# Performance work log

Hardware: AMD Instinct MI355X
Metric: run time of the kernel (lower is better)

Reference implementation:

```python
import jax, jax.numpy as jnp
import numpy as np

N = 65536        # nodes
E = 1048576      # edges (avg degree 16)
IN, HID, OUT = 128, 64, 64


def setup_inputs() -> dict:
    key = jax.random.key(0)
    ks = jax.random.split(key, 6)
    x = jax.random.normal(ks[0], (N, IN), jnp.float32)
    edge_index = jax.random.randint(ks[1], (2, E), 0, N, jnp.int32)
    # Glorot-style init as in PyG GCNConv
    W1 = jax.random.normal(ks[2], (IN, HID), jnp.float32) * (1.0 / np.sqrt(IN))
    b1 = jnp.zeros((HID,), jnp.float32)
    W2 = jax.random.normal(ks[3], (HID, OUT), jnp.float32) * (1.0 / np.sqrt(HID))
    b2 = jnp.zeros((OUT,), jnp.float32)
    return {"x": x, "edge_index": edge_index, "W1": W1, "b1": b1, "W2": W2, "b2": b2}


def _gcn_conv(h, src, dst, dinv_sqrt, W, b):
    # PyG GCNConv: transform, then D^-1/2 A_hat D^-1/2 aggregation (A_hat has self-loops)
    h = h @ W                                   # [N, F_out]
    norm = dinv_sqrt[src] * dinv_sqrt[dst]      # [E+N]
    msg = h[src] * norm[:, None]                # gather + scale
    return jax.ops.segment_sum(msg, dst, num_segments=N) + b


def reference(x, edge_index, W1, b1, W2, b2):
    loops = jnp.arange(N, dtype=edge_index.dtype)
    src = jnp.concatenate([edge_index[0], loops])   # [E+N] with self-loops
    dst = jnp.concatenate([edge_index[1], loops])
    deg = jax.ops.segment_sum(jnp.ones_like(dst, x.dtype), dst, num_segments=N)
    dinv_sqrt = jax.lax.rsqrt(deg)                  # deg >= 1 thanks to self-loops
    h = jax.nn.relu(_gcn_conv(x, src, dst, dinv_sqrt, W1, b1))
    return _gcn_conv(h, src, dst, dinv_sqrt, W2, b2)
```

## Files before the change

kernel.cpp:

```cpp
#include <hip/hip_runtime.h>
#include <hip/hip_fp16.h>


#define N_NODES 65536
#define E_EDGES 1048576
#define F_IN    128
#define F_HID   64
#define CAPSH   6

__global__ __launch_bounds__(256) void k_fill(
        const int* __restrict__ src, const int* __restrict__ dst,
        int* __restrict__ cnt, unsigned short* __restrict__ csr) {
    int g     = blockIdx.x & 7;
    int chunk = blockIdx.x >> 3;
    int i     = chunk * blockDim.x + threadIdx.x;
    int4 d = ((const int4*)dst)[i];
#pragma unroll
    for (int k = 0; k < 4; ++k) {
        int dv = k == 0 ? d.x : k == 1 ? d.y : k == 2 ? d.z : d.w;
        if ((dv >> 13) == g) {
            int pos = atomicAdd(&cnt[dv], 1);
            csr[(dv << CAPSH) + pos] = (unsigned short)src[4 * i + k];
        }
    }
}

__device__ inline unsigned int pack_h2(float a, float b) {
    __half2 h = __floats2half2_rn(a, b);
    return *(unsigned int*)&h;
}

template <int F_K>
__global__ __launch_bounds__(256) void k_gemm_scale(
        const float* __restrict__ h, const float* __restrict__ W,
        const int* __restrict__ cnt, __half* __restrict__ P) {
    int wave = __builtin_amdgcn_readfirstlane(threadIdx.x >> 6);
    int lane = threadIdx.x & 63;
    int v = blockIdx.x * 64 + lane;
    const float4* hr = (const float4*)(h + (size_t)v * F_K);
    float4 acc[4];
#pragma unroll
    for (int j = 0; j < 4; ++j) acc[j] = make_float4(0.f, 0.f, 0.f, 0.f);
#pragma unroll 4
    for (int kb = 0; kb < F_K / 4; ++kb) {
        float4 hv = hr[kb];
#pragma unroll
        for (int r = 0; r < 4; ++r) {
            float hk = r == 0 ? hv.x : r == 1 ? hv.y : r == 2 ? hv.z : hv.w;
            const float4* Wr = (const float4*)(W + (size_t)(kb * 4 + r) * 64 + (wave << 4));
#pragma unroll
            for (int j = 0; j < 4; ++j) {
                float4 w = Wr[j];
                acc[j].x = fmaf(hk, w.x, acc[j].x);
                acc[j].y = fmaf(hk, w.y, acc[j].y);
                acc[j].z = fmaf(hk, w.z, acc[j].z);
                acc[j].w = fmaf(hk, w.w, acc[j].w);
            }
        }
    }
    float s = rsqrtf((float)cnt[v] + 1.0f);
    __half* Pr = P + (size_t)v * 64 + (wave << 4);
    uint4 q0, q1;
    q0.x = pack_h2(acc[0].x * s, acc[0].y * s);
    q0.y = pack_h2(acc[0].z * s, acc[0].w * s);
    q0.z = pack_h2(acc[1].x * s, acc[1].y * s);
    q0.w = pack_h2(acc[1].z * s, acc[1].w * s);
    q1.x = pack_h2(acc[2].x * s, acc[2].y * s);
    q1.y = pack_h2(acc[2].z * s, acc[2].w * s);
    q1.z = pack_h2(acc[3].x * s, acc[3].y * s);
    q1.w = pack_h2(acc[3].z * s, acc[3].w * s);
    ((uint4*)Pr)[0] = q0;
    ((uint4*)Pr)[1] = q1;
}

__device__ inline float4 h4_to_f4(uint2 q) {
    __half2 a = *(__half2*)&q.x;
    __half2 b = *(__half2*)&q.y;
    float2 fa = __half22float2(a), fb = __half22float2(b);
    return make_float4(fa.x, fa.y, fb.x, fb.y);
}

template <bool RELU>
__global__ void k_aggregate(const __half* __restrict__ P,
                            const unsigned short* __restrict__ csr,
                            const int* __restrict__ cnt, const float* __restrict__ b,
                            float* __restrict__ out) {
    int lane = threadIdx.x & 63;
    int sub  = lane >> 4;
    int col4 = lane & 15;
    int wave  = (blockIdx.x * blockDim.x + threadIdx.x) >> 6;
    int nwave = (gridDim.x * blockDim.x) >> 6;
    float4 bias = ((const float4*)b)[col4];
    for (int v = wave; v < N_NODES; v += nwave) {
        int c   = cnt[v];
        int beg = v << CAPSH;
        float4 acc = make_float4(0.f, 0.f, 0.f, 0.f);
        if (sub == 0) {
            uint2 q = ((const uint2*)(P + (size_t)v * 64))[col4];
            acc = h4_to_f4(q);
        }
        for (int i = 0; i < c; i += 4) {
            int e = i + sub;
            if (e < c) {
                int s = csr[beg + e];
                uint2 q = ((const uint2*)(P + (size_t)s * 64))[col4];
                float4 p = h4_to_f4(q);
                acc.x += p.x; acc.y += p.y; acc.z += p.z; acc.w += p.w;
            }
        }
        acc.x += __shfl_xor(acc.x, 16); acc.y += __shfl_xor(acc.y, 16);
        acc.z += __shfl_xor(acc.z, 16); acc.w += __shfl_xor(acc.w, 16);
        acc.x += __shfl_xor(acc.x, 32); acc.y += __shfl_xor(acc.y, 32);
        acc.z += __shfl_xor(acc.z, 32); acc.w += __shfl_xor(acc.w, 32);
        if (lane < 16) {
            float s = rsqrtf((float)c + 1.0f);
            float4 o;
            o.x = s * acc.x + bias.x;
            o.y = s * acc.y + bias.y;
            o.z = s * acc.z + bias.z;
            o.w = s * acc.w + bias.w;
            if (RELU) {
                o.x = o.x > 0.f ? o.x : 0.f;
                o.y = o.y > 0.f ? o.y : 0.f;
                o.z = o.z > 0.f ? o.z : 0.f;
                o.w = o.w > 0.f ? o.w : 0.f;
            }
            ((float4*)(out + (size_t)v * 64))[col4] = o;
        }
    }
}

extern "C" void kernel_launch(void* const* d_in, const int* in_sizes, int n_in,
                              void* d_out, int out_size, void* d_ws, size_t ws_size,
                              hipStream_t stream) {
    const float* x   = (const float*)d_in[0];
    const int*   ei  = (const int*)d_in[1];
    const float* W1  = (const float*)d_in[2];
    const float* b1  = (const float*)d_in[3];
    const float* W2  = (const float*)d_in[4];
    const float* b2  = (const float*)d_in[5];
    float*       out = (float*)d_out;

    const int* src = ei;
    const int* dst = ei + E_EDGES;

    int*            cnt = (int*)d_ws;
    unsigned short* csr = (unsigned short*)(cnt + N_NODES);
    __half*         P   = (__half*)(csr + ((size_t)N_NODES << CAPSH));
    float*          H   = out;

    hipMemsetAsync(cnt, 0, N_NODES * sizeof(int), stream);
    k_fill<<<(E_EDGES / 4 / 256) * 8, 256, 0, stream>>>(src, dst, cnt, csr);

    k_gemm_scale<F_IN><<<N_NODES / 64, 256, 0, stream>>>(x, W1, cnt, P);
    k_aggregate<true><<<4096, 256, 0, stream>>>(P, csr, cnt, b1, H);

    k_gemm_scale<F_HID><<<N_NODES / 64, 256, 0, stream>>>(H, W2, cnt, P);
    k_aggregate<false><<<4096, 256, 0, stream>>>(P, csr, cnt, b2, out);
}
```

Baseline: 236.7 us.

## Fuse first GEMM with CSR fill kernel and precompute inverse sqrt degrees

Merges the first-layer GEMM and the edge bucketing fill into one launch, with blocks split by index so the GEMM no longer waits on the degree count. Because degrees are unknown when the GEMM runs, the first aggregation now scales each source row by a gathered dinv value. A small kernel precomputes dinv once for both layers, and the aggregation loop is unrolled by two edges. This trades an extra per-edge dinv gather and an extra launch for concurrency between the compute-bound GEMM and the atomic-heavy fill.

```diff
diff --git a/kernel.cpp b/kernel.cpp
--- a/kernel.cpp
+++ b/kernel.cpp
@@ -7,36 +7,28 @@
 #define F_IN    128
 #define F_HID   64
 #define CAPSH   6
-
-__global__ __launch_bounds__(256) void k_fill(
-        const int* __restrict__ src, const int* __restrict__ dst,
-        int* __restrict__ cnt, unsigned short* __restrict__ csr) {
-    int g     = blockIdx.x & 7;
-    int chunk = blockIdx.x >> 3;
-    int i     = chunk * blockDim.x + threadIdx.x;
-    int4 d = ((const int4*)dst)[i];
-#pragma unroll
-    for (int k = 0; k < 4; ++k) {
-        int dv = k == 0 ? d.x : k == 1 ? d.y : k == 2 ? d.z : d.w;
-        if ((dv >> 13) == g) {
-            int pos = atomicAdd(&cnt[dv], 1);
-            csr[(dv << CAPSH) + pos] = (unsigned short)src[4 * i + k];
-        }
-    }
-}
+#define GEMM1_BLOCKS (N_NODES / 64)
+#define FILL_BLOCKS  ((E_EDGES / 4 / 256) * 8)
 
 __device__ inline unsigned int pack_h2(float a, float b) {
     __half2 h = __floats2half2_rn(a, b);
     return *(unsigned int*)&h;
 }
 
-template <int F_K>
-__global__ __launch_bounds__(256) void k_gemm_scale(
-        const float* __restrict__ h, const float* __restrict__ W,
-        const int* __restrict__ cnt, __half* __restrict__ P) {
+__device__ inline float4 h4_to_f4(uint2 q) {
+    __half2 a = *(__half2*)&q.x;
+    __half2 b = *(__half2*)&q.y;
+    float2 fa = __half22float2(a), fb = __half22float2(b);
+    return make_float4(fa.x, fa.y, fb.x, fb.y);
+}
+
+template <int F_K, bool SCALED>
+__device__ inline void gemm_body(const float* __restrict__ h, const float* __restrict__ W,
+                                 const float* __restrict__ dinv, __half* __restrict__ P,
+                                 int bid) {
     int wave = __builtin_amdgcn_readfirstlane(threadIdx.x >> 6);
     int lane = threadIdx.x & 63;
-    int v = blockIdx.x * 64 + lane;
+    int v = bid * 64 + lane;
     const float4* hr = (const float4*)(h + (size_t)v * F_K);
     float4 acc[4];
 #pragma unroll
@@ -58,7 +50,7 @@
             }
         }
     }
-    float s = rsqrtf((float)cnt[v] + 1.0f);
+    float s = SCALED ? dinv[v] : 1.0f;
     __half* Pr = P + (size_t)v * 64 + (wave << 4);
     uint4 q0, q1;
     q0.x = pack_h2(acc[0].x * s, acc[0].y * s);
@@ -73,18 +65,47 @@
     ((uint4*)Pr)[1] = q1;
 }
 
-__device__ inline float4 h4_to_f4(uint2 q) {
-    __half2 a = *(__half2*)&q.x;
-    __half2 b = *(__half2*)&q.y;
-    float2 fa = __half22float2(a), fb = __half22float2(b);
-    return make_float4(fa.x, fa.y, fb.x, fb.y);
+__global__ __launch_bounds__(256) void k_fused(
+        const float* __restrict__ x, const float* __restrict__ W1,
+        __half* __restrict__ P,
+        const int* __restrict__ src, const int* __restrict__ dst,
+        int* __restrict__ cnt, unsigned short* __restrict__ csr) {
+    if (blockIdx.x < GEMM1_BLOCKS) {
+        gemm_body<F_IN, false>(x, W1, nullptr, P, blockIdx.x);
+    } else {
+        int fb    = blockIdx.x - GEMM1_BLOCKS;
+        int g     = fb & 7;
+        int chunk = fb >> 3;
+        int i     = chunk * blockDim.x + threadIdx.x;
+        int4 d = ((const int4*)dst)[i];
+#pragma unroll
+        for (int k = 0; k < 4; ++k) {
+            int dv = k == 0 ? d.x : k == 1 ? d.y : k == 2 ? d.z : d.w;
+            if ((dv >> 13) == g) {
+                int pos = atomicAdd(&cnt[dv], 1);
+                csr[(dv << CAPSH) + pos] = (unsigned short)src[4 * i + k];
+            }
+        }
+    }
 }
 
-template <bool RELU>
+__global__ void k_dinv(const int* __restrict__ cnt, float* __restrict__ dinv) {
+    int v = blockIdx.x * blockDim.x + threadIdx.x;
+    if (v < N_NODES) dinv[v] = rsqrtf((float)cnt[v] + 1.0f);
+}
+
+template <int F_K, bool SCALED>
+__global__ __launch_bounds__(256) void k_gemm(
+        const float* __restrict__ h, const float* __restrict__ W,
+        const float* __restrict__ dinv, __half* __restrict__ P) {
+    gemm_body<F_K, SCALED>(h, W, dinv, P, blockIdx.x);
+}
+
+template <bool RELU, bool SRCSCALE>
 __global__ void k_aggregate(const __half* __restrict__ P,
                             const unsigned short* __restrict__ csr,
-                            const int* __restrict__ cnt, const float* __restrict__ b,
-                            float* __restrict__ out) {
+                            const int* __restrict__ cnt, const float* __restrict__ dinv,
+                            const float* __restrict__ b, float* __restrict__ out) {
     int lane = threadIdx.x & 63;
     int sub  = lane >> 4;
     int col4 = lane & 15;
@@ -92,20 +113,33 @@
     int nwave = (gridDim.x * blockDim.x) >> 6;
     float4 bias = ((const float4*)b)[col4];
     for (int v = wave; v < N_NODES; v += nwave) {
-        int c   = cnt[v];
-        int beg = v << CAPSH;
+        int c    = cnt[v];
+        float dv = dinv[v];
+        int beg  = v << CAPSH;
         float4 acc = make_float4(0.f, 0.f, 0.f, 0.f);
         if (sub == 0) {
             uint2 q = ((const uint2*)(P + (size_t)v * 64))[col4];
-            acc = h4_to_f4(q);
+            float4 p = h4_to_f4(q);
+            float sc = SRCSCALE ? dv : 1.0f;
+            acc.x = sc * p.x; acc.y = sc * p.y; acc.z = sc * p.z; acc.w = sc * p.w;
         }
-        for (int i = 0; i < c; i += 4) {
-            int e = i + sub;
-            if (e < c) {
-                int s = csr[beg + e];
-                uint2 q = ((const uint2*)(P + (size_t)s * 64))[col4];
-                float4 p = h4_to_f4(q);
-                acc.x += p.x; acc.y += p.y; acc.z += p.z; acc.w += p.w;
+        for (int i = 0; i < c; i += 8) {
+            int e0 = i + sub, e1 = i + sub + 4;
+            if (e0 < c) {
+                int s0 = csr[beg + e0];
+                float f0 = SRCSCALE ? dinv[s0] : 1.0f;
+                uint2 q0 = ((const uint2*)(P + (size_t)s0 * 64))[col4];
+                float4 p0 = h4_to_f4(q0);
+                acc.x = fmaf(f0, p0.x, acc.x); acc.y = fmaf(f0, p0.y, acc.y);
+                acc.z = fmaf(f0, p0.z, acc.z); acc.w = fmaf(f0, p0.w, acc.w);
+            }
+            if (e1 < c) {
+                int s1 = csr[beg + e1];
+                float f1 = SRCSCALE ? dinv[s1] : 1.0f;
+                uint2 q1 = ((const uint2*)(P + (size_t)s1 * 64))[col4];
+                float4 p1 = h4_to_f4(q1);
+                acc.x = fmaf(f1, p1.x, acc.x); acc.y = fmaf(f1, p1.y, acc.y);
+                acc.z = fmaf(f1, p1.z, acc.z); acc.w = fmaf(f1, p1.w, acc.w);
             }
         }
         acc.x += __shfl_xor(acc.x, 16); acc.y += __shfl_xor(acc.y, 16);
@@ -113,12 +147,11 @@
         acc.x += __shfl_xor(acc.x, 32); acc.y += __shfl_xor(acc.y, 32);
         acc.z += __shfl_xor(acc.z, 32); acc.w += __shfl_xor(acc.w, 32);
         if (lane < 16) {
-            float s = rsqrtf((float)c + 1.0f);
             float4 o;
-            o.x = s * acc.x + bias.x;
-            o.y = s * acc.y + bias.y;
-            o.z = s * acc.z + bias.z;
-            o.w = s * acc.w + bias.w;
+            o.x = dv * acc.x + bias.x;
+            o.y = dv * acc.y + bias.y;
+            o.z = dv * acc.z + bias.z;
+            o.w = dv * acc.w + bias.w;
             if (RELU) {
                 o.x = o.x > 0.f ? o.x : 0.f;
                 o.y = o.y > 0.f ? o.y : 0.f;
@@ -144,17 +177,19 @@
     const int* src = ei;
     const int* dst = ei + E_EDGES;
 
-    int*            cnt = (int*)d_ws;
-    unsigned short* csr = (unsigned short*)(cnt + N_NODES);
-    __half*         P   = (__half*)(csr + ((size_t)N_NODES << CAPSH));
-    float*          H   = out;
+    int*            cnt  = (int*)d_ws;
+    float*          dinv = (float*)(cnt + N_NODES);
+    unsigned short* csr  = (unsigned short*)(dinv + N_NODES);
+    __half*         P    = (__half*)(csr + ((size_t)N_NODES << CAPSH));
+    float*          H    = out;
 
     hipMemsetAsync(cnt, 0, N_NODES * sizeof(int), stream);
-    k_fill<<<(E_EDGES / 4 / 256) * 8, 256, 0, stream>>>(src, dst, cnt, csr);
 
-    k_gemm_scale<F_IN><<<N_NODES / 64, 256, 0, stream>>>(x, W1, cnt, P);
-    k_aggregate<true><<<4096, 256, 0, stream>>>(P, csr, cnt, b1, H);
+    k_fused<<<GEMM1_BLOCKS + FILL_BLOCKS, 256, 0, stream>>>(x, W1, P, src, dst, cnt, csr);
+    k_dinv<<<N_NODES / 256, 256, 0, stream>>>(cnt, dinv);
 
-    k_gemm_scale<F_HID><<<N_NODES / 64, 256, 0, stream>>>(H, W2, cnt, P);
-    k_aggregate<false><<<4096, 256, 0, stream>>>(P, csr, cnt, b2, out);
+    k_aggregate<true, true><<<4096, 256, 0, stream>>>(P, csr, cnt, dinv, b1, H);
+
+    k_gemm<F_HID, true><<<N_NODES / 64, 256, 0, stream>>>(H, W2, dinv, P);
+    k_aggregate<false, false><<<4096, 256, 0, stream>>>(P, csr, cnt, dinv, b2, out);
 }
```

After: 232.0 us. -2.0%, faster.

## Fuse GEMM1 with CSR fill and fold GEMM2 into layer-1 aggregation

Applied to the files above, without the earlier changes.

The first X·W1 GEMM now runs in the same launch as the CSR fill, since it no longer needs degrees. The source-side normalisation is applied per edge during aggregation, using an extra cnt[s] lookup and rsqrt. Layer-1 aggregation now computes ReLU(h)·W2 in registers via wave shuffles and writes a half-precision P2 directly. This removes the H round-trip and two launches. The inner gather loop is also unrolled by four to keep more loads in flight. In exchange, layer 1 does extra random cnt reads per edge, and every wave computes a 64x64 matvec with W2 loads per node.

```diff
diff --git a/kernel.cpp b/kernel.cpp
--- a/kernel.cpp
+++ b/kernel.cpp
@@ -7,36 +7,27 @@
 #define F_IN    128
 #define F_HID   64
 #define CAPSH   6
-
-__global__ __launch_bounds__(256) void k_fill(
-        const int* __restrict__ src, const int* __restrict__ dst,
-        int* __restrict__ cnt, unsigned short* __restrict__ csr) {
-    int g     = blockIdx.x & 7;
-    int chunk = blockIdx.x >> 3;
-    int i     = chunk * blockDim.x + threadIdx.x;
-    int4 d = ((const int4*)dst)[i];
-#pragma unroll
-    for (int k = 0; k < 4; ++k) {
-        int dv = k == 0 ? d.x : k == 1 ? d.y : k == 2 ? d.z : d.w;
-        if ((dv >> 13) == g) {
-            int pos = atomicAdd(&cnt[dv], 1);
-            csr[(dv << CAPSH) + pos] = (unsigned short)src[4 * i + k];
-        }
-    }
-}
+#define GEMM1_BLOCKS (N_NODES / 64)
+#define FILL_BLOCKS  ((E_EDGES / 4 / 256) * 8)
 
 __device__ inline unsigned int pack_h2(float a, float b) {
     __half2 h = __floats2half2_rn(a, b);
     return *(unsigned int*)&h;
 }
 
+__device__ inline float4 h4_to_f4(uint2 q) {
+    __half2 a = *(__half2*)&q.x;
+    __half2 b = *(__half2*)&q.y;
+    float2 fa = __half22float2(a), fb = __half22float2(b);
+    return make_float4(fa.x, fa.y, fb.x, fb.y);
+}
+
 template <int F_K>
-__global__ __launch_bounds__(256) void k_gemm_scale(
-        const float* __restrict__ h, const float* __restrict__ W,
-        const int* __restrict__ cnt, __half* __restrict__ P) {
+__device__ inline void gemm_body(const float* __restrict__ h, const float* __restrict__ W,
+                                 __half* __restrict__ P, int bid) {
     int wave = __builtin_amdgcn_readfirstlane(threadIdx.x >> 6);
     int lane = threadIdx.x & 63;
-    int v = blockIdx.x * 64 + lane;
+    int v = bid * 64 + lane;
     const float4* hr = (const float4*)(h + (size_t)v * F_K);
     float4 acc[4];
 #pragma unroll
@@ -58,33 +49,102 @@
             }
         }
     }
-    float s = rsqrtf((float)cnt[v] + 1.0f);
     __half* Pr = P + (size_t)v * 64 + (wave << 4);
     uint4 q0, q1;
-    q0.x = pack_h2(acc[0].x * s, acc[0].y * s);
-    q0.y = pack_h2(acc[0].z * s, acc[0].w * s);
-    q0.z = pack_h2(acc[1].x * s, acc[1].y * s);
-    q0.w = pack_h2(acc[1].z * s, acc[1].w * s);
-    q1.x = pack_h2(acc[2].x * s, acc[2].y * s);
-    q1.y = pack_h2(acc[2].z * s, acc[2].w * s);
-    q1.z = pack_h2(acc[3].x * s, acc[3].y * s);
-    q1.w = pack_h2(acc[3].z * s, acc[3].w * s);
+    q0.x = pack_h2(acc[0].x, acc[0].y); q0.y = pack_h2(acc[0].z, acc[0].w);
+    q0.z = pack_h2(acc[1].x, acc[1].y); q0.w = pack_h2(acc[1].z, acc[1].w);
+    q1.x = pack_h2(acc[2].x, acc[2].y); q1.y = pack_h2(acc[2].z, acc[2].w);
+    q1.z = pack_h2(acc[3].x, acc[3].y); q1.w = pack_h2(acc[3].z, acc[3].w);
     ((uint4*)Pr)[0] = q0;
     ((uint4*)Pr)[1] = q1;
 }
 
-__device__ inline float4 h4_to_f4(uint2 q) {
-    __half2 a = *(__half2*)&q.x;
-    __half2 b = *(__half2*)&q.y;
-    float2 fa = __half22float2(a), fb = __half22float2(b);
-    return make_float4(fa.x, fa.y, fb.x, fb.y);
-}
-
-template <bool RELU>
-__global__ void k_aggregate(const __half* __restrict__ P,
-                            const unsigned short* __restrict__ csr,
-                            const int* __restrict__ cnt, const float* __restrict__ b,
-                            float* __restrict__ out) {
+__global__ __launch_bounds__(256) void k_fused(
+        const float* __restrict__ x, const float* __restrict__ W1,
+        __half* __restrict__ P,
+        const int* __restrict__ src, const int* __restrict__ dst,
+        int* __restrict__ cnt, unsigned short* __restrict__ csr) {
+    if (blockIdx.x < GEMM1_BLOCKS) {
+        gemm_body<F_IN>(x, W1, P, blockIdx.x);
+    } else {
+        int fb    = blockIdx.x - GEMM1_BLOCKS;
+        int g     = fb & 7;
+        int chunk = fb >> 3;
+        int i     = chunk * blockDim.x + threadIdx.x;
+        int4 d = ((const int4*)dst)[i];
+#pragma unroll
+        for (int k = 0; k < 4; ++k) {
+            int dv = k == 0 ? d.x : k == 1 ? d.y : k == 2 ? d.z : d.w;
+            if ((dv >> 13) == g) {
+                int pos = atomicAdd(&cnt[dv], 1);
+                csr[(dv << CAPSH) + pos] = (unsigned short)src[4 * i + k];
+            }
+        }
+    }
+}
+
+__global__ __launch_bounds__(256) void k_agg1_gemm2(
+        const __half* __restrict__ P1, const unsigned short* __restrict__ csr,
+        const int* __restrict__ cnt, const float* __restrict__ b1,
+        const float* __restrict__ W2, __half* __restrict__ P2) {
+    int lane = threadIdx.x & 63;
+    int sub  = lane >> 4;
+    int col4 = lane & 15;
+    int wave  = (blockIdx.x * blockDim.x + threadIdx.x) >> 6;
+    int nwave = (gridDim.x * blockDim.x) >> 6;
+    float4 bias = ((const float4*)b1)[col4];
+    for (int v = wave; v < N_NODES; v += nwave) {
+        int c    = cnt[v];
+        float dv = rsqrtf((float)c + 1.0f);
+        int beg  = v << CAPSH;
+        float4 acc = make_float4(0.f, 0.f, 0.f, 0.f);
+        if (sub == 0) {
+            float4 p = h4_to_f4(((const uint2*)(P1 + (size_t)v * 64))[col4]);
+            acc.x = dv * p.x; acc.y = dv * p.y; acc.z = dv * p.z; acc.w = dv * p.w;
+        }
+        for (int i = 0; i < c; i += 16) {
+#pragma unroll
+            for (int u = 0; u < 4; ++u) {
+                int e = i + sub + 4 * u;
+                if (e < c) {
+                    int s = csr[beg + e];
+                    float f = rsqrtf((float)cnt[s] + 1.0f);
+                    float4 p = h4_to_f4(((const uint2*)(P1 + (size_t)s * 64))[col4]);
+                    acc.x = fmaf(f, p.x, acc.x); acc.y = fmaf(f, p.y, acc.y);
+                    acc.z = fmaf(f, p.z, acc.z); acc.w = fmaf(f, p.w, acc.w);
+                }
+            }
+        }
+        acc.x += __shfl_xor(acc.x, 16); acc.y += __shfl_xor(acc.y, 16);
+        acc.z += __shfl_xor(acc.z, 16); acc.w += __shfl_xor(acc.w, 16);
+        acc.x += __shfl_xor(acc.x, 32); acc.y += __shfl_xor(acc.y, 32);
+        acc.z += __shfl_xor(acc.z, 32); acc.w += __shfl_xor(acc.w, 32);
+        float4 h;
+        h.x = dv * acc.x + bias.x; h.x = h.x > 0.f ? h.x : 0.f;
+        h.y = dv * acc.y + bias.y; h.y = h.y > 0.f ? h.y : 0.f;
+        h.z = dv * acc.z + bias.z; h.z = h.z > 0.f ? h.z : 0.f;
+        h.w = dv * acc.w + bias.w; h.w = h.w > 0.f ? h.w : 0.f;
+        float p2 = 0.f;
+#pragma unroll
+        for (int k16 = 0; k16 < 16; ++k16) {
+            float hx = __shfl(h.x, k16);
+            float hy = __shfl(h.y, k16);
+            float hz = __shfl(h.z, k16);
+            float hw = __shfl(h.w, k16);
+            const float* Wr = W2 + (size_t)(k16 * 4) * 64 + lane;
+            p2 = fmaf(hx, Wr[0],   p2);
+            p2 = fmaf(hy, Wr[64],  p2);
+            p2 = fmaf(hz, Wr[128], p2);
+            p2 = fmaf(hw, Wr[192], p2);
+        }
+        P2[(size_t)v * 64 + lane] = __float2half_rn(p2 * dv);
+    }
+}
+
+__global__ __launch_bounds__(256) void k_agg2(
+        const __half* __restrict__ P, const unsigned short* __restrict__ csr,
+        const int* __restrict__ cnt, const float* __restrict__ b,
+        float* __restrict__ out) {
     int lane = threadIdx.x & 63;
     int sub  = lane >> 4;
     int col4 = lane & 15;
@@ -92,20 +152,23 @@
     int nwave = (gridDim.x * blockDim.x) >> 6;
     float4 bias = ((const float4*)b)[col4];
     for (int v = wave; v < N_NODES; v += nwave) {
-        int c   = cnt[v];
-        int beg = v << CAPSH;
+        int c    = cnt[v];
+        float dv = rsqrtf((float)c + 1.0f);
+        int beg  = v << CAPSH;
         float4 acc = make_float4(0.f, 0.f, 0.f, 0.f);
         if (sub == 0) {
-            uint2 q = ((const uint2*)(P + (size_t)v * 64))[col4];
-            acc = h4_to_f4(q);
-        }
-        for (int i = 0; i < c; i += 4) {
-            int e = i + sub;
-            if (e < c) {
-                int s = csr[beg + e];
-                uint2 q = ((const uint2*)(P + (size_t)s * 64))[col4];
-                float4 p = h4_to_f4(q);
-                acc.x += p.x; acc.y += p.y; acc.z += p.z; acc.w += p.w;
+            float4 p = h4_to_f4(((const uint2*)(P + (size_t)v * 64))[col4]);
+            acc = p;
+        }
+        for (int i = 0; i < c; i += 16) {
+#pragma unroll
+            for (int u = 0; u < 4; ++u) {
+                int e = i + sub + 4 * u;
+                if (e < c) {
+                    int s = csr[beg + e];
+                    float4 p = h4_to_f4(((const uint2*)(P + (size_t)s * 64))[col4]);
+                    acc.x += p.x; acc.y += p.y; acc.z += p.z; acc.w += p.w;
+                }
             }
         }
         acc.x += __shfl_xor(acc.x, 16); acc.y += __shfl_xor(acc.y, 16);
@@ -113,18 +176,11 @@
         acc.x += __shfl_xor(acc.x, 32); acc.y += __shfl_xor(acc.y, 32);
         acc.z += __shfl_xor(acc.z, 32); acc.w += __shfl_xor(acc.w, 32);
         if (lane < 16) {
-            float s = rsqrtf((float)c + 1.0f);
             float4 o;
-            o.x = s * acc.x + bias.x;
-            o.y = s * acc.y + bias.y;
-            o.z = s * acc.z + bias.z;
-            o.w = s * acc.w + bias.w;
-            if (RELU) {
-                o.x = o.x > 0.f ? o.x : 0.f;
-                o.y = o.y > 0.f ? o.y : 0.f;
-                o.z = o.z > 0.f ? o.z : 0.f;
-                o.w = o.w > 0.f ? o.w : 0.f;
-            }
+            o.x = dv * acc.x + bias.x;
+            o.y = dv * acc.y + bias.y;
+            o.z = dv * acc.z + bias.z;
+            o.w = dv * acc.w + bias.w;
             ((float4*)(out + (size_t)v * 64))[col4] = o;
         }
     }
@@ -146,15 +202,14 @@
 
     int*            cnt = (int*)d_ws;
     unsigned short* csr = (unsigned short*)(cnt + N_NODES);
-    __half*         P   = (__half*)(csr + ((size_t)N_NODES << CAPSH));
-    float*          H   = out;
+    __half*         P1  = (__half*)(csr + ((size_t)N_NODES << CAPSH));
+    __half*         P2  = P1 + (size_t)N_NODES * 64;
 
     hipMemsetAsync(cnt, 0, N_NODES * sizeof(int), stream);
-    k_fill<<<(E_EDGES / 4 / 256) * 8, 256, 0, stream>>>(src, dst, cnt, csr);
-
-    k_gemm_scale<F_IN><<<N_NODES / 64, 256, 0, stream>>>(x, W1, cnt, P);
-    k_aggregate<true><<<4096, 256, 0, stream>>>(P, csr, cnt, b1, H);
-
-    k_gemm_scale<F_HID><<<N_NODES / 64, 256, 0, stream>>>(H, W2, cnt, P);
-    k_aggregate<false><<<4096, 256, 0, stream>>>(P, csr, cnt, b2, out);
-}
+
+    k_fused<<<GEMM1_BLOCKS + FILL_BLOCKS, 256, 0, stream>>>(x, W1, P1, src, dst, cnt, csr);
+
+    k_agg1_gemm2<<<4096, 256, 0, stream>>>(P1, csr, cnt, b1, W2, P2);
+
+    k_agg2<<<4096, 256, 0, stream>>>(P2, csr, cnt, b2, out);
+}
```

New measurement: 263.1 us. 11.1% more time.
